# Optimization experiments

Measured on AMD Instinct MI355X. Metric: run time of the kernel, lower is better.

Reference implementation:

```python
import jax, jax.numpy as jnp
import numpy as np

B, S, ENC, HID = 2, 2048, 2048, 2048
HQ, HKV, D = 8, 4, 256
SOFTCAP = 50.0
SCALING = float(256) ** -0.5  # query_pre_attn_scalar ** -0.5
EPS = 1e-6
NEG = -1e9  # finite stand-in for -inf in additive masks


def _rms_norm(x, w, eps=EPS):
    # GemmaRMSNorm: fp32 compute, scale by (1 + weight)
    xf = x.astype(jnp.float32)
    n = xf * jax.lax.rsqrt(jnp.mean(xf * xf, axis=-1, keepdims=True) + eps)
    return (n * (1.0 + w.astype(jnp.float32))).astype(x.dtype)


def _rotate_half(x):
    x1, x2 = jnp.split(x, 2, axis=-1)
    return jnp.concatenate([-x2, x1], axis=-1)


def _apply_rope(q, k, cos, sin):
    # q,k: [B, H, S, D]; cos,sin: [1, S, D] -> unsqueeze head dim
    c, s = cos[:, None, :, :], sin[:, None, :, :]
    return q * c + _rotate_half(q) * s, k * c + _rotate_half(k) * s


def setup_inputs() -> dict:
    key = jax.random.key(0)
    ks = jax.random.split(key, 8)
    hidden_states = jax.random.normal(ks[0], (B, S, HID), jnp.float32)
    encoder_hidden_states = jax.random.normal(ks[1], (B, ENC, HID), jnp.float32)
    # RoPE tables (base 10000)
    pos = jnp.arange(S, dtype=jnp.float32)
    inv_freq = 1.0 / (10000.0 ** (jnp.arange(0, D, 2, dtype=jnp.float32) / D))
    freqs = pos[:, None] * inv_freq[None, :]                 # [S, D/2]
    emb = jnp.concatenate([freqs, freqs], axis=-1)           # [S, D]
    cos = jnp.cos(emb)[None]                                 # [1, S, D]
    sin = jnp.sin(emb)[None]
    # merged additive mask: causal over self part, fully visible cross part
    causal = jnp.where(jnp.arange(S)[:, None] >= jnp.arange(S)[None, :], 0.0, NEG)
    mask = jnp.concatenate([causal, jnp.zeros((S, ENC), jnp.float32)], axis=-1)
    merged_attention_mask = mask[None, None].astype(jnp.float32)  # [1,1,S,S+ENC]
    w = 0.02
    Wq = jax.random.normal(ks[2], (HQ * D, HID), jnp.float32) * w
    Wk = jax.random.normal(ks[3], (HKV * D, HID), jnp.float32) * w
    Wv = jax.random.normal(ks[4], (HKV * D, HID), jnp.float32) * w
    Wo = jax.random.normal(ks[5], (HID, HQ * D), jnp.float32) * w
    q_norm_w = jnp.zeros((D,), jnp.float32)
    k_norm_w = jnp.zeros((D,), jnp.float32)
    return dict(hidden_states=hidden_states, encoder_hidden_states=encoder_hidden_states,
                cos=cos, sin=sin, merged_attention_mask=merged_attention_mask,
                Wq=Wq, Wk=Wk, Wv=Wv, Wo=Wo, q_norm_w=q_norm_w, k_norm_w=k_norm_w)


def reference(hidden_states, encoder_hidden_states, cos, sin, merged_attention_mask,
              Wq, Wk, Wv, Wo, q_norm_w, k_norm_w):
    b, s, _ = hidden_states.shape
    enc = encoder_hidden_states.shape[1]
    n_rep = HQ // HKV
    # projections
    q = hidden_states @ Wq.T                                 # [B,S,HQ*D]
    k_self = hidden_states @ Wk.T
    v_self = hidden_states @ Wv.T
    k_cross = encoder_hidden_states @ Wk.T
    v_cross = encoder_hidden_states @ Wv.T
    q = q.reshape(b, s, HQ, D).transpose(0, 2, 1, 3)         # [B,HQ,S,D]
    k_self = k_self.reshape(b, s, HKV, D).transpose(0, 2, 1, 3)
    v_self = v_self.reshape(b, s, HKV, D).transpose(0, 2, 1, 3)
    k_cross = k_cross.reshape(b, enc, HKV, D).transpose(0, 2, 1, 3)
    v_cross = v_cross.reshape(b, enc, HKV, D).transpose(0, 2, 1, 3)
    # QK RMSNorm + RoPE (RoPE only on self q/k)
    q = _rms_norm(q, q_norm_w)
    k_self = _rms_norm(k_self, k_norm_w)
    k_cross = _rms_norm(k_cross, k_norm_w)
    q, k_self = _apply_rope(q, k_self, cos, sin)
    # merged KV + GQA repeat
    k = jnp.concatenate([k_self, k_cross], axis=2)           # [B,HKV,S+ENC,D]
    v = jnp.concatenate([v_self, v_cross], axis=2)
    k = jnp.repeat(k, n_rep, axis=1)                         # [B,HQ,S+ENC,D]
    v = jnp.repeat(v, n_rep, axis=1)
    # eager softcapped attention
    scores = jnp.einsum('bhqd,bhkd->bhqk', q, k) * SCALING
    scores = SOFTCAP * jnp.tanh(scores / SOFTCAP)
    scores = scores + merged_attention_mask
    probs = jax.nn.softmax(scores, axis=-1)
    attn = jnp.einsum('bhqk,bhkd->bhqd', probs, v)           # [B,HQ,S,D]
    attn = attn.transpose(0, 2, 1, 3).reshape(b, s, HQ * D)
    return attn @ Wo.T
```

## Files before the change

kernel.cpp:

```cpp
#include <hip/hip_runtime.h>
#include <cstdint>

typedef __attribute__((ext_vector_type(8))) short bf16x8;
typedef __attribute__((ext_vector_type(4))) float f32x4;

#define B_ 2
#define S_ 2048
#define ENC_ 2048
#define HID_ 2048
#define HQ_ 8
#define HKV_ 4
#define D_ 256
#define L_ 4096

__device__ __forceinline__ short f2bf(float f) {
  uint32_t u = __builtin_bit_cast(uint32_t, f);
  u = (u + 0x7fffu + ((u >> 16) & 1u)) >> 16;
  return (short)u;
}
__device__ __forceinline__ float bf2f(short s) {
  uint32_t u = ((uint32_t)(uint16_t)s) << 16;
  return __builtin_bit_cast(float, u);
}

__device__ __forceinline__ void llds16(const void* g, void* s) {
  __builtin_amdgcn_global_load_lds(
      (const __attribute__((address_space(1))) void*)(__builtin_bit_cast(uintptr_t, g)),
      (__attribute__((address_space(3))) void*)(uint32_t)(__builtin_bit_cast(uintptr_t, s)),
      16, 0, 0);
}

__device__ __forceinline__ void wg_barrier() {
  asm volatile("" ::: "memory");
  __builtin_amdgcn_s_barrier();
  asm volatile("" ::: "memory");
}

__global__ __launch_bounds__(256) void cvt_f32_bf16(const float* __restrict__ in,
                                                    short* __restrict__ out, int n) {
  int i = (blockIdx.x * 256 + threadIdx.x) * 4;
  if (i >= n) return;
  float4 v = *(const float4*)(in + i);
  short4 r;
  r.x = f2bf(v.x); r.y = f2bf(v.y); r.z = f2bf(v.z); r.w = f2bf(v.w);
  *(short4*)(out + i) = r;
}

template <int BF16OUT>
__global__ __launch_bounds__(256, 2)
void gemm_bt(const short* __restrict__ A, const short* __restrict__ Bw,
             void* __restrict__ Cout, int M, int N, int K) {
  __shared__ __align__(16) short As[128 * 32];
  __shared__ __align__(16) short Bs[128 * 32];
  const int t = threadIdx.x;
  const int w = t >> 6;
  const int l = t & 63;
  const int lr = l & 15;
  const int lq = l >> 4;
  const int bm = blockIdx.y * 128;
  const int bn = blockIdx.x * 128;
  const int wm = (w & 1) * 64;
  const int wn = (w >> 1) * 64;

  f32x4 acc[4][4];
#pragma unroll
  for (int i = 0; i < 4; i++)
#pragma unroll
    for (int j = 0; j < 4; j++) acc[i][j] = f32x4{0.f, 0.f, 0.f, 0.f};

  const int srow = 32 * w + (l >> 2);
  const int scol = (l & 3) * 8;
  const short* gA = A + (size_t)(bm + srow) * K + scol;
  const short* gB = Bw + (size_t)(bn + srow) * K + scol;
  short* sA = &As[srow * 32 + scol];
  short* sB = &Bs[srow * 32 + scol];

  for (int k0 = 0; k0 < K; k0 += 32) {
    llds16(gA + k0, sA);
    llds16(gA + k0 + (size_t)16 * K, sA + 16 * 32);
    llds16(gB + k0, sB);
    llds16(gB + k0 + (size_t)16 * K, sB + 16 * 32);
    __syncthreads();
    bf16x8 af[4], bfr[4];
#pragma unroll
    for (int mi = 0; mi < 4; mi++)
      af[mi] = *(const bf16x8*)&As[(wm + 16 * mi + lr) * 32 + lq * 8];
#pragma unroll
    for (int ni = 0; ni < 4; ni++)
      bfr[ni] = *(const bf16x8*)&Bs[(wn + 16 * ni + lr) * 32 + lq * 8];
    __syncthreads();
#pragma unroll
    for (int mi = 0; mi < 4; mi++)
#pragma unroll
      for (int ni = 0; ni < 4; ni++)
        acc[mi][ni] =
            __builtin_amdgcn_mfma_f32_16x16x32_bf16(af[mi], bfr[ni], acc[mi][ni], 0, 0, 0);
  }

#pragma unroll
  for (int mi = 0; mi < 4; mi++)
#pragma unroll
    for (int ni = 0; ni < 4; ni++)
#pragma unroll
      for (int r = 0; r < 4; r++) {
        int row = bm + wm + 16 * mi + lq * 4 + r;
        int col = bn + wn + 16 * ni + lr;
        float v = acc[mi][ni][r];
        if (BF16OUT)
          ((short*)Cout)[(size_t)row * N + col] = f2bf(v);
        else
          ((float*)Cout)[(size_t)row * N + col] = v;
      }
}

__global__ __launch_bounds__(256)
void norm_rope(const short* __restrict__ src, int src_ld, int col0, int H,
               short* __restrict__ dst, int dstL, int pos_off, int do_rope, int kswz,
               const float* __restrict__ wn, const float* __restrict__ cosp,
               const float* __restrict__ sinp) {
  __shared__ float sh[256];
  __shared__ float red[4];
  int bid = blockIdx.x;
  int s = bid & (S_ - 1);
  int h = (bid >> 11) % H;
  int b = (bid >> 11) / H;
  int d = threadIdx.x;
  int w = d >> 6, l = d & 63;
  float x = bf2f(src[(size_t)(b * S_ + s) * src_ld + col0 + h * D_ + d]);
  float ss = x * x;
#pragma unroll
  for (int off = 32; off; off >>= 1) ss += __shfl_xor(ss, off, 64);
  if (l == 0) red[w] = ss;
  __syncthreads();
  float tot = red[0] + red[1] + red[2] + red[3];
  float y = x * rsqrtf(tot * (1.0f / D_) + 1e-6f) * (1.0f + wn[d]);
  float outv = y;
  if (do_rope) {
    sh[d] = y;
    __syncthreads();
    float c = cosp[s * D_ + d];
    float sn = sinp[s * D_ + d];
    outv = (d < 128) ? (y * c - sh[d + 128] * sn) : (y * c + sh[d - 128] * sn);
  }
  int dd = d;
  if (kswz) dd = (((d >> 3) ^ (s & 7)) << 3) | (d & 7);
  dst[((size_t)(b * H + h) * dstL + pos_off + s) * D_ + dd] = f2bf(outv);
}

__global__ __launch_bounds__(256)
void v_transpose(const short* __restrict__ qkv_self, const short* __restrict__ kv_cross,
                 short* __restrict__ Vt) {
  __shared__ __align__(16) short tile[64][72];
  int bid = blockIdx.x;
  int dt = bid & 3;
  int lt = (bid >> 2) & 63;
  int h = (bid >> 8) & 3;
  int b = bid >> 10;
  int t = threadIdx.x;
  int rl = t >> 2;
  int cc = (t & 3) * 16;
  int l = lt * 64 + rl;
  const short* src;
  if (lt < 32)
    src = qkv_self + (size_t)(b * S_ + l) * 4096 + 3072 + h * D_ + dt * 64 + cc;
  else
    src = kv_cross + (size_t)(b * ENC_ + (l - S_)) * 2048 + 1024 + h * D_ + dt * 64 + cc;
  *(bf16x8*)&tile[rl][cc] = *(const bf16x8*)src;
  *(bf16x8*)&tile[rl][cc + 8] = *(const bf16x8*)(src + 8);
  __syncthreads();
  int dl = t >> 2;
  int lc = (t & 3) * 16;
  bf16x8 v0, v1;
#pragma unroll
  for (int j = 0; j < 8; j++) {
    v0[j] = tile[lc + j][dl];
    v1[j] = tile[lc + 8 + j][dl];
  }
  int d = dt * 64 + dl;
  int e3 = dl & 3;
  int c0 = 2 * (t & 3);
  int c1 = c0 + 1;
  int p0 = (c0 & 4) | ((c0 ^ e3) & 3);
  int p1 = (c1 & 4) | ((c1 ^ e3) & 3);
  short* rowp = Vt + ((size_t)(b * HKV_ + h) * D_ + d) * (size_t)L_ + lt * 64;
  *(bf16x8*)(rowp + p0 * 8) = v0;
  *(bf16x8*)(rowp + p1 * 8) = v1;
}

__global__ __launch_bounds__(256)
void flash_attn(const short* __restrict__ Q, const short* __restrict__ K,
                const short* __restrict__ Vt, short* __restrict__ part0,
                short* __restrict__ part1, float* __restrict__ lsum) {
  __shared__ __align__(16) short Ks[2][32 * 256];
  __shared__ __align__(16) short Vs[2][256 * 32];
  __shared__ __align__(16) short Ps[4][16 * 40];
  int t = threadIdx.x, w = t >> 6, l = t & 63;
  int lr = l & 15, lq = l >> 4, x7 = lr & 7, x3 = lr & 3;
  int bid = blockIdx.x;
  int pair = bid >> 5;
  int p = (bid >> 4) & 1;
  int bh = bid & 15;
  int b = bh >> 3, h = bh & 7, hk = h >> 1;
  short* op = p ? part1 : part0;

  const short* Kbase = K + (size_t)(b * HKV_ + hk) * L_ * D_;
  const short* Vbase = Vt + (size_t)(b * HKV_ + hk) * (size_t)D_ * L_;

  auto stage = [&](int bufi, int k0) {
    const short* kg = Kbase + (size_t)(k0 + 8 * w + (l >> 5)) * 256 + (l & 31) * 8;
    short* ks = &Ks[bufi][8 * w * 256 + l * 8];
#pragma unroll
    for (int i = 0; i < 4; i++) llds16(kg + i * 512, ks + i * 512);
    const short* vg = Vbase + (size_t)(64 * w + (l >> 2)) * (size_t)L_ + k0 + (l & 3) * 8;
    short* vs = &Vs[bufi][64 * w * 32 + l * 8];
#pragma unroll
    for (int i = 0; i < 4; i++) llds16(vg + (size_t)(16 * i) * L_, vs + i * 512);
  };

  int gi = p;
  const int lenA = pair + 33;

  for (int phase = 0; phase < 2; ++phase) {
    int qt = phase ? (31 - pair) : pair;
    int q0 = qt * 64;
    int nself = qt + 1;
    int base = phase ? lenA : 0;
    int lim = base + nself + 32;
    int qglob = q0 + 16 * w + lr;

    bf16x8 qf[8];
    {
      const short* qb = Q + ((size_t)(b * HQ_ + h) * S_ + qglob) * D_ + lq * 8;
#pragma unroll
      for (int kf = 0; kf < 8; kf++) qf[kf] = *(const bf16x8*)(qb + kf * 32);
    }
    f32x4 o[16];
#pragma unroll
    for (int i = 0; i < 16; i++) o[i] = f32x4{0.f, 0.f, 0.f, 0.f};
    float lacc = 0.f;

    int gcur = gi, u = 0, buf = 0;
    {
      int local = gcur - base;
      int j = (local < nself) ? local : (local - nself + 32);
      stage(0, j * 64);
    }

    while (true) {
      int gn = gcur, un = u + 1;
      if (un == 2) { un = 0; gn = gcur + 2; }
      bool hn = (gn < lim);
      if (hn) {
        int localn = gn - base;
        int jn = (localn < nself) ? localn : (localn - nself + 32);
        stage(buf ^ 1, jn * 64 + 32 * un);
        asm volatile("s_waitcnt vmcnt(8)" ::: "memory");
      } else {
        asm volatile("s_waitcnt vmcnt(0)" ::: "memory");
      }
      wg_barrier();

      int local = gcur - base;
      int j = (local < nself) ? local : (local - nself + 32);
      int k0 = j * 64 + 32 * u;
      bool diag = (j == qt);
      const short* KsB = &Ks[buf][0];
      const short* VsB = &Vs[buf][0];

      f32x4 sc[2];
      sc[0] = f32x4{0.f, 0.f, 0.f, 0.f};
      sc[1] = f32x4{0.f, 0.f, 0.f, 0.f};
      __builtin_amdgcn_s_setprio(1);
#pragma unroll
      for (int kf = 0; kf < 8; kf++) {
#pragma unroll
        for (int nt = 0; nt < 2; nt++) {
          bf16x8 a = *(const bf16x8*)&KsB[(nt * 16 + lr) * 256 + (((4 * kf + lq) ^ x7) * 8)];
          sc[nt] = __builtin_amdgcn_mfma_f32_16x16x32_bf16(a, qf[kf], sc[nt], 0, 0, 0);
        }
      }
      __builtin_amdgcn_s_setprio(0);

#pragma unroll
      for (int nt = 0; nt < 2; nt++) {
        float pe[4];
#pragma unroll
        for (int r = 0; r < 4; r++) {
          float s = sc[nt][r];
          float t2 = s * s * 1.5625e-6f;
          float hh = fmaf(t2, -0.0033730157f, 0.0083333338f);
          hh = fmaf(t2, hh, -0.020833334f);
          hh = fmaf(t2, hh, 0.0625f);
          float cap = s * hh;
          float pv = __expf(cap);
          if (diag && (k0 + nt * 16 + 4 * lq + r > qglob)) pv = 0.f;
          pe[r] = pv;
        }
        lacc += (pe[0] + pe[1]) + (pe[2] + pe[3]);
        uint32_t lo = (uint32_t)(uint16_t)f2bf(pe[0]) | ((uint32_t)(uint16_t)f2bf(pe[1]) << 16);
        uint32_t hi = (uint32_t)(uint16_t)f2bf(pe[2]) | ((uint32_t)(uint16_t)f2bf(pe[3]) << 16);
        *(uint2*)&Ps[w][lr * 40 + nt * 16 + lq * 4] = uint2{lo, hi};
      }

      bf16x8 pb = *(const bf16x8*)&Ps[w][lr * 40 + lq * 8];
      __builtin_amdgcn_s_setprio(1);
#pragma unroll
      for (int dt = 0; dt < 16; dt++) {
        bf16x8 va = *(const bf16x8*)&VsB[(dt * 16 + lr) * 32 + ((lq ^ x3) * 8)];
        o[dt] = __builtin_amdgcn_mfma_f32_16x16x32_bf16(va, pb, o[dt], 0, 0, 0);
      }
      __builtin_amdgcn_s_setprio(0);

      wg_barrier();
      if (!hn) break;
      gcur = gn; u = un; buf ^= 1;
    }
    gi = gcur + 2;

    size_t orow = ((size_t)b * S_ + qglob) * (HQ_ * D_) + h * D_;
#pragma unroll
    for (int dt = 0; dt < 16; dt++) {
      short4 st;
      st.x = f2bf(o[dt][0]);
      st.y = f2bf(o[dt][1]);
      st.z = f2bf(o[dt][2]);
      st.w = f2bf(o[dt][3]);
      *(short4*)(op + orow + dt * 16 + 4 * lq) = st;
    }
    float lrow = lacc;
    lrow += __shfl_xor(lrow, 16, 64);
    lrow += __shfl_xor(lrow, 32, 64);
    if (lq == 0)
      lsum[(((size_t)p * B_ + b) * HQ_ + h) * S_ + qglob] = lrow;
  }
}

__global__ __launch_bounds__(256)
void combine2(const short* __restrict__ p0, const short* __restrict__ p1,
              const float* __restrict__ lsum, short* __restrict__ out) {
  int tid = blockIdx.x * 256 + threadIdx.x;
  int flat = tid * 4;
  int h = (flat >> 8) & 7;
  int s = (flat >> 11) & 2047;
  int b = flat >> 22;
  size_t sbase = ((size_t)b * HQ_ + h) * S_ + s;
  const size_t SP = (size_t)B_ * HQ_ * S_;
  float inv = 1.0f / (lsum[sbase] + lsum[SP + sbase]);
  short4 a = *(const short4*)(p0 + (size_t)flat);
  short4 c = *(const short4*)(p1 + (size_t)flat);
  short4 r;
  r.x = f2bf((bf2f(a.x) + bf2f(c.x)) * inv);
  r.y = f2bf((bf2f(a.y) + bf2f(c.y)) * inv);
  r.z = f2bf((bf2f(a.z) + bf2f(c.z)) * inv);
  r.w = f2bf((bf2f(a.w) + bf2f(c.w)) * inv);
  *(short4*)(out + flat) = r;
}

extern "C" void kernel_launch(void* const* d_in, const int* in_sizes, int n_in, void* d_out,
                              int out_size, void* d_ws, size_t ws_size, hipStream_t stream) {
  (void)in_sizes; (void)n_in; (void)out_size; (void)ws_size;
  const float* hidden = (const float*)d_in[0];
  const float* encoder = (const float*)d_in[1];
  const float* cosp = (const float*)d_in[2];
  const float* sinp = (const float*)d_in[3];
  const float* Wq = (const float*)d_in[5];
  const float* Wk = (const float*)d_in[6];
  const float* Wv = (const float*)d_in[7];
  const float* Wo = (const float*)d_in[8];
  const float* qnw = (const float*)d_in[9];
  const float* knw = (const float*)d_in[10];

  short* ws = (short*)d_ws;
  short* hs_bf = ws;
  short* enc_bf = ws + 8388608;
  short* wqkv_bf = ws + 16777216;
  short* wo_bf = ws + 25165824;
  short* qkv_self = ws + 29360128;
  short* kv_cross = ws + 46137344;
  short* Kb = ws + 54525952;
  short* Vtb = ws + 62914560;
  short* attn_b = hs_bf;
  short* Qb = enc_bf;
  short* part0 = qkv_self;
  short* part1 = qkv_self + 8388608;
  float* lsum = (float*)d_out;

  cvt_f32_bf16<<<8192, 256, 0, stream>>>(hidden, hs_bf, 8388608);
  cvt_f32_bf16<<<8192, 256, 0, stream>>>(encoder, enc_bf, 8388608);
  cvt_f32_bf16<<<4096, 256, 0, stream>>>(Wq, wqkv_bf, 4194304);
  cvt_f32_bf16<<<2048, 256, 0, stream>>>(Wk, wqkv_bf + 4194304, 2097152);
  cvt_f32_bf16<<<2048, 256, 0, stream>>>(Wv, wqkv_bf + 6291456, 2097152);
  cvt_f32_bf16<<<4096, 256, 0, stream>>>(Wo, wo_bf, 4194304);

  gemm_bt<1><<<dim3(32, 32), 256, 0, stream>>>(hs_bf, wqkv_bf, qkv_self, 4096, 4096, 2048);
  gemm_bt<1><<<dim3(16, 32), 256, 0, stream>>>(enc_bf, wqkv_bf + (size_t)2048 * 2048, kv_cross,
                                               4096, 2048, 2048);

  norm_rope<<<32768, 256, 0, stream>>>(qkv_self, 4096, 0, 8, Qb, 2048, 0, 1, 0, qnw, cosp, sinp);
  norm_rope<<<16384, 256, 0, stream>>>(qkv_self, 4096, 2048, 4, Kb, 4096, 0, 1, 1, knw, cosp, sinp);
  norm_rope<<<16384, 256, 0, stream>>>(kv_cross, 2048, 0, 4, Kb, 4096, 2048, 0, 1, knw, cosp, sinp);

  v_transpose<<<2048, 256, 0, stream>>>(qkv_self, kv_cross, Vtb);

  flash_attn<<<512, 256, 0, stream>>>(Qb, Kb, Vtb, part0, part1, lsum);
  combine2<<<8192, 256, 0, stream>>>(part0, part1, lsum, attn_b);

  gemm_bt<0><<<dim3(16, 32), 256, 0, stream>>>(attn_b, wo_bf, d_out, 4096, 2048, 2048);
}
```

Baseline: 585.7 us.

## Process two query sub-tiles per wave and split KV four ways in flash attention

Result: no change. 584.5 us (-0.2%).

```diff
diff --git a/kernel.cpp b/kernel.cpp
--- a/kernel.cpp
+++ b/kernel.cpp
@@ -177,7 +177,7 @@
     v1[j] = tile[lc + 8 + j][dl];
   }
   int d = dt * 64 + dl;
-  int e3 = dl & 3;
+  int e3 = (dl >> 1) & 3;
   int c0 = 2 * (t & 3);
   int c1 = c0 + 1;
   int p0 = (c0 & 4) | ((c0 ^ e3) & 3);
@@ -187,21 +187,22 @@
   *(bf16x8*)(rowp + p1 * 8) = v1;
 }
 
-__global__ __launch_bounds__(256)
+__global__ __launch_bounds__(256, 2)
 void flash_attn(const short* __restrict__ Q, const short* __restrict__ K,
                 const short* __restrict__ Vt, short* __restrict__ part0,
-                short* __restrict__ part1, float* __restrict__ lsum) {
+                short* __restrict__ part1, short* __restrict__ part2,
+                short* __restrict__ part3, float* __restrict__ lsum) {
   __shared__ __align__(16) short Ks[2][32 * 256];
   __shared__ __align__(16) short Vs[2][256 * 32];
-  __shared__ __align__(16) short Ps[4][16 * 40];
+  __shared__ __align__(16) short Ps[4][2][16 * 40];
   int t = threadIdx.x, w = t >> 6, l = t & 63;
-  int lr = l & 15, lq = l >> 4, x7 = lr & 7, x3 = lr & 3;
+  int lr = l & 15, lq = l >> 4, x7 = lr & 7, vx = (lr >> 1) & 3;
   int bid = blockIdx.x;
-  int pair = bid >> 5;
-  int p = (bid >> 4) & 1;
+  int pair = bid >> 6;
+  int p = (bid >> 4) & 3;
   int bh = bid & 15;
   int b = bh >> 3, h = bh & 7, hk = h >> 1;
-  short* op = p ? part1 : part0;
+  short* op = (p == 0) ? part0 : (p == 1) ? part1 : (p == 2) ? part2 : part3;
 
   const short* Kbase = K + (size_t)(b * HKV_ + hk) * L_ * D_;
   const short* Vbase = Vt + (size_t)(b * HKV_ + hk) * (size_t)D_ * L_;
@@ -218,26 +219,34 @@
   };
 
   int gi = p;
-  const int lenA = pair + 33;
+  const int lenA = 2 * pair + 34;
 
   for (int phase = 0; phase < 2; ++phase) {
-    int qt = phase ? (31 - pair) : pair;
-    int q0 = qt * 64;
-    int nself = qt + 1;
+    int qt = phase ? (15 - pair) : pair;
+    int q0 = qt * 128;
+    int nself = 2 * qt + 2;
     int base = phase ? lenA : 0;
     int lim = base + nself + 32;
-    int qglob = q0 + 16 * w + lr;
-
-    bf16x8 qf[8];
+    int qg0 = q0 + 32 * w + lr;
+    int qg1 = qg0 + 16;
+
+    bf16x8 qf0[8], qf1[8];
     {
-      const short* qb = Q + ((size_t)(b * HQ_ + h) * S_ + qglob) * D_ + lq * 8;
-#pragma unroll
-      for (int kf = 0; kf < 8; kf++) qf[kf] = *(const bf16x8*)(qb + kf * 32);
-    }
-    f32x4 o[16];
-#pragma unroll
-    for (int i = 0; i < 16; i++) o[i] = f32x4{0.f, 0.f, 0.f, 0.f};
-    float lacc = 0.f;
+      const short* qb0 = Q + ((size_t)(b * HQ_ + h) * S_ + qg0) * D_ + lq * 8;
+      const short* qb1 = qb0 + (size_t)16 * D_;
+#pragma unroll
+      for (int kf = 0; kf < 8; kf++) {
+        qf0[kf] = *(const bf16x8*)(qb0 + kf * 32);
+        qf1[kf] = *(const bf16x8*)(qb1 + kf * 32);
+      }
+    }
+    f32x4 o0[16], o1[16];
+#pragma unroll
+    for (int i = 0; i < 16; i++) {
+      o0[i] = f32x4{0.f, 0.f, 0.f, 0.f};
+      o1[i] = f32x4{0.f, 0.f, 0.f, 0.f};
+    }
+    float lacc0 = 0.f, lacc1 = 0.f;
 
     int gcur = gi, u = 0, buf = 0;
     {
@@ -248,7 +257,7 @@
 
     while (true) {
       int gn = gcur, un = u + 1;
-      if (un == 2) { un = 0; gn = gcur + 2; }
+      if (un == 2) { un = 0; gn = gcur + 4; }
       bool hn = (gn < lim);
       if (hn) {
         int localn = gn - base;
@@ -263,51 +272,61 @@
       int local = gcur - base;
       int j = (local < nself) ? local : (local - nself + 32);
       int k0 = j * 64 + 32 * u;
-      bool diag = (j == qt);
+      bool diag = (local >= nself - 2) && (local < nself);
       const short* KsB = &Ks[buf][0];
       const short* VsB = &Vs[buf][0];
 
-      f32x4 sc[2];
-      sc[0] = f32x4{0.f, 0.f, 0.f, 0.f};
-      sc[1] = f32x4{0.f, 0.f, 0.f, 0.f};
+      f32x4 sc[2][2];
+#pragma unroll
+      for (int nt = 0; nt < 2; nt++) {
+        sc[nt][0] = f32x4{0.f, 0.f, 0.f, 0.f};
+        sc[nt][1] = f32x4{0.f, 0.f, 0.f, 0.f};
+      }
       __builtin_amdgcn_s_setprio(1);
 #pragma unroll
       for (int kf = 0; kf < 8; kf++) {
 #pragma unroll
         for (int nt = 0; nt < 2; nt++) {
           bf16x8 a = *(const bf16x8*)&KsB[(nt * 16 + lr) * 256 + (((4 * kf + lq) ^ x7) * 8)];
-          sc[nt] = __builtin_amdgcn_mfma_f32_16x16x32_bf16(a, qf[kf], sc[nt], 0, 0, 0);
+          sc[nt][0] = __builtin_amdgcn_mfma_f32_16x16x32_bf16(a, qf0[kf], sc[nt][0], 0, 0, 0);
+          sc[nt][1] = __builtin_amdgcn_mfma_f32_16x16x32_bf16(a, qf1[kf], sc[nt][1], 0, 0, 0);
         }
       }
       __builtin_amdgcn_s_setprio(0);
 
-#pragma unroll
-      for (int nt = 0; nt < 2; nt++) {
+      auto softcap_store = [&](const f32x4& s4, int keybase, int qg, float& lacc,
+                               int qh, int nt) {
         float pe[4];
 #pragma unroll
         for (int r = 0; r < 4; r++) {
-          float s = sc[nt][r];
+          float s = s4[r];
           float t2 = s * s * 1.5625e-6f;
           float hh = fmaf(t2, -0.0033730157f, 0.0083333338f);
           hh = fmaf(t2, hh, -0.020833334f);
           hh = fmaf(t2, hh, 0.0625f);
           float cap = s * hh;
           float pv = __expf(cap);
-          if (diag && (k0 + nt * 16 + 4 * lq + r > qglob)) pv = 0.f;
+          if (diag && (keybase + 4 * lq + r > qg)) pv = 0.f;
           pe[r] = pv;
         }
         lacc += (pe[0] + pe[1]) + (pe[2] + pe[3]);
         uint32_t lo = (uint32_t)(uint16_t)f2bf(pe[0]) | ((uint32_t)(uint16_t)f2bf(pe[1]) << 16);
         uint32_t hi = (uint32_t)(uint16_t)f2bf(pe[2]) | ((uint32_t)(uint16_t)f2bf(pe[3]) << 16);
-        *(uint2*)&Ps[w][lr * 40 + nt * 16 + lq * 4] = uint2{lo, hi};
-      }
-
-      bf16x8 pb = *(const bf16x8*)&Ps[w][lr * 40 + lq * 8];
+        *(uint2*)&Ps[w][qh][lr * 40 + nt * 16 + lq * 4] = uint2{lo, hi};
+      };
+      softcap_store(sc[0][0], k0, qg0, lacc0, 0, 0);
+      softcap_store(sc[1][0], k0 + 16, qg0, lacc0, 0, 1);
+      softcap_store(sc[0][1], k0, qg1, lacc1, 1, 0);
+      softcap_store(sc[1][1], k0 + 16, qg1, lacc1, 1, 1);
+
+      bf16x8 pb0 = *(const bf16x8*)&Ps[w][0][lr * 40 + lq * 8];
+      bf16x8 pb1 = *(const bf16x8*)&Ps[w][1][lr * 40 + lq * 8];
       __builtin_amdgcn_s_setprio(1);
 #pragma unroll
       for (int dt = 0; dt < 16; dt++) {
-        bf16x8 va = *(const bf16x8*)&VsB[(dt * 16 + lr) * 32 + ((lq ^ x3) * 8)];
-        o[dt] = __builtin_amdgcn_mfma_f32_16x16x32_bf16(va, pb, o[dt], 0, 0, 0);
+        bf16x8 va = *(const bf16x8*)&VsB[(dt * 16 + lr) * 32 + ((lq ^ vx) * 8)];
+        o0[dt] = __builtin_amdgcn_mfma_f32_16x16x32_bf16(va, pb0, o0[dt], 0, 0, 0);
+        o1[dt] = __builtin_amdgcn_mfma_f32_16x16x32_bf16(va, pb1, o1[dt], 0, 0, 0);
       }
       __builtin_amdgcn_s_setprio(0);
 
@@ -315,44 +334,59 @@
       if (!hn) break;
       gcur = gn; u = un; buf ^= 1;
     }
-    gi = gcur + 2;
-
-    size_t orow = ((size_t)b * S_ + qglob) * (HQ_ * D_) + h * D_;
+    gi = gcur + 4;
+
+    size_t orow0 = ((size_t)b * S_ + qg0) * (HQ_ * D_) + h * D_;
+    size_t orow1 = orow0 + (size_t)16 * (HQ_ * D_);
 #pragma unroll
     for (int dt = 0; dt < 16; dt++) {
       short4 st;
-      st.x = f2bf(o[dt][0]);
-      st.y = f2bf(o[dt][1]);
-      st.z = f2bf(o[dt][2]);
-      st.w = f2bf(o[dt][3]);
-      *(short4*)(op + orow + dt * 16 + 4 * lq) = st;
-    }
-    float lrow = lacc;
-    lrow += __shfl_xor(lrow, 16, 64);
-    lrow += __shfl_xor(lrow, 32, 64);
-    if (lq == 0)
-      lsum[(((size_t)p * B_ + b) * HQ_ + h) * S_ + qglob] = lrow;
+      st.x = f2bf(o0[dt][0]);
+      st.y = f2bf(o0[dt][1]);
+      st.z = f2bf(o0[dt][2]);
+      st.w = f2bf(o0[dt][3]);
+      *(short4*)(op + orow0 + dt * 16 + 4 * lq) = st;
+      st.x = f2bf(o1[dt][0]);
+      st.y = f2bf(o1[dt][1]);
+      st.z = f2bf(o1[dt][2]);
+      st.w = f2bf(o1[dt][3]);
+      *(short4*)(op + orow1 + dt * 16 + 4 * lq) = st;
+    }
+    float lrow0 = lacc0, lrow1 = lacc1;
+    lrow0 += __shfl_xor(lrow0, 16, 64);
+    lrow0 += __shfl_xor(lrow0, 32, 64);
+    lrow1 += __shfl_xor(lrow1, 16, 64);
+    lrow1 += __shfl_xor(lrow1, 32, 64);
+    if (lq == 0) {
+      size_t lb = (((size_t)p * B_ + b) * HQ_ + h) * S_;
+      lsum[lb + qg0] = lrow0;
+      lsum[lb + qg1] = lrow1;
+    }
   }
 }
 
 __global__ __launch_bounds__(256)
-void combine2(const short* __restrict__ p0, const short* __restrict__ p1,
+void combine4(const short* __restrict__ p0, const short* __restrict__ p1,
+              const short* __restrict__ p2, const short* __restrict__ p3,
               const float* __restrict__ lsum, short* __restrict__ out) {
   int tid = blockIdx.x * 256 + threadIdx.x;
-  int flat = tid * 4;
-  int h = (flat >> 8) & 7;
-  int s = (flat >> 11) & 2047;
-  int b = flat >> 22;
+  size_t flat = (size_t)tid * 4;
+  int h = ((int)(flat >> 8)) & 7;
+  int s = ((int)(flat >> 11)) & 2047;
+  int b = (int)(flat >> 22);
   size_t sbase = ((size_t)b * HQ_ + h) * S_ + s;
   const size_t SP = (size_t)B_ * HQ_ * S_;
-  float inv = 1.0f / (lsum[sbase] + lsum[SP + sbase]);
-  short4 a = *(const short4*)(p0 + (size_t)flat);
-  short4 c = *(const short4*)(p1 + (size_t)flat);
+  float inv = 1.0f / (lsum[sbase] + lsum[SP + sbase] + lsum[2 * SP + sbase] +
+                      lsum[3 * SP + sbase]);
+  short4 a = *(const short4*)(p0 + flat);
+  short4 c = *(const short4*)(p1 + flat);
+  short4 d = *(const short4*)(p2 + flat);
+  short4 e = *(const short4*)(p3 + flat);
   short4 r;
-  r.x = f2bf((bf2f(a.x) + bf2f(c.x)) * inv);
-  r.y = f2bf((bf2f(a.y) + bf2f(c.y)) * inv);
-  r.z = f2bf((bf2f(a.z) + bf2f(c.z)) * inv);
-  r.w = f2bf((bf2f(a.w) + bf2f(c.w)) * inv);
+  r.x = f2bf((bf2f(a.x) + bf2f(c.x) + bf2f(d.x) + bf2f(e.x)) * inv);
+  r.y = f2bf((bf2f(a.y) + bf2f(c.y) + bf2f(d.y) + bf2f(e.y)) * inv);
+  r.z = f2bf((bf2f(a.z) + bf2f(c.z) + bf2f(d.z) + bf2f(e.z)) * inv);
+  r.w = f2bf((bf2f(a.w) + bf2f(c.w) + bf2f(d.w) + bf2f(e.w)) * inv);
   *(short4*)(out + flat) = r;
 }
 
@@ -383,6 +417,8 @@
   short* Qb = enc_bf;
   short* part0 = qkv_self;
   short* part1 = qkv_self + 8388608;
+  short* part2 = kv_cross;
+  short* part3 = wqkv_bf;
   float* lsum = (float*)d_out;
 
   cvt_f32_bf16<<<8192, 256, 0, stream>>>(hidden, hs_bf, 8388608);
@@ -402,8 +438,8 @@
 
   v_transpose<<<2048, 256, 0, stream>>>(qkv_self, kv_cross, Vtb);
 
-  flash_attn<<<512, 256, 0, stream>>>(Qb, Kb, Vtb, part0, part1, lsum);
-  combine2<<<8192, 256, 0, stream>>>(part0, part1, lsum, attn_b);
+  flash_attn<<<512, 256, 0, stream>>>(Qb, Kb, Vtb, part0, part1, part2, part3, lsum);
+  combine4<<<16384, 256, 0, stream>>>(part0, part1, part2, part3, lsum, attn_b);
 
   gemm_bt<0><<<dim3(16, 32), 256, 0, stream>>>(attn_b, wo_bf, d_out, 4096, 2048, 2048);
 }
```
